# Kernel tuning notes

Hardware: AMD Instinct MI355X
Metric: run time of the kernel (lower is better)

The kernel has to match this reference:

```python
import jax, jax.numpy as jnp
import numpy as np

B, T, N, C = 2, 3, 6, 16            # batch, time steps, cameras, frustum channels
FD, FH, FW = 48, 24, 64             # frustum depth bins, feature height, width
GX, GY, GZ = 100, 100, 8            # voxel grid size (X, Y, Z)
PC_MIN = np.array([-50.0, -50.0, -3.0], np.float32)
PC_MAX = np.array([50.0, 50.0, 5.0], np.float32)
D_MIN, D_MAX = 2.0, 46.8            # uniform depth discretization (UD)
OUT_CH = 40


def setup_inputs() -> dict:
    key = jax.random.key(0)
    ks = jax.random.split(key, 8)
    frustum_features = jax.random.normal(ks[0], (B, T, N, C, FD, FH, FW), jnp.float32)
    # camera looks along world +x so voxel points land in front of the camera
    base_rt = jnp.array([[0., -1., 0., 0.],
                         [0., 0., -1., 0.],
                         [1., 0., 0., 0.],
                         [0., 0., 0., 1.]], jnp.float32)
    RT = base_rt + 0.02 * jax.random.normal(ks[1], (B, T, N, 4, 4), jnp.float32)
    K = jnp.array([[32., 0., FW / 2.], [0., 32., FH / 2.], [0., 0., 1.]], jnp.float32)
    intrins = K + 0.1 * jax.random.normal(ks[2], (B, 3, 3), jnp.float32)
    DoF = jnp.eye(4, dtype=jnp.float32) + 0.01 * jax.random.normal(ks[3], (B, T, 4, 4), jnp.float32)
    W_N = 0.05 * jax.random.normal(ks[4], (OUT_CH, N * C), jnp.float32)
    b_N = jnp.zeros((OUT_CH,), jnp.float32)
    W_T = 0.05 * jax.random.normal(ks[5], (OUT_CH, T * OUT_CH), jnp.float32)
    b_T = jnp.zeros((OUT_CH,), jnp.float32)
    return {"frustum_features": frustum_features, "RT": RT, "intrins": intrins,
            "DoF": DoF, "W_N": W_N, "b_N": b_N, "W_T": W_T, "b_T": b_T}


def _grid_sample_3d(feat, grid):
    """Trilinear grid_sample. feat [M,C,D,H,W], grid [M,A,B2,C3,3] with
    normalized (x->W, y->H, z->D) coords, align_corners=True, zeros padding."""
    def one(f, g):
        _, Dd, Hh, Ww = f.shape
        ix = (g[..., 0] + 1.) * 0.5 * (Ww - 1)
        iy = (g[..., 1] + 1.) * 0.5 * (Hh - 1)
        iz = (g[..., 2] + 1.) * 0.5 * (Dd - 1)
        x0 = jnp.floor(ix); y0 = jnp.floor(iy); z0 = jnp.floor(iz)
        wx1 = ix - x0; wy1 = iy - y0; wz1 = iz - z0
        wx0 = 1. - wx1; wy0 = 1. - wy1; wz0 = 1. - wz1

        def corner(zf, yf, xf, w):
            valid = ((xf >= 0) & (xf <= Ww - 1) & (yf >= 0) & (yf <= Hh - 1)
                     & (zf >= 0) & (zf <= Dd - 1))
            zi = jnp.clip(zf, 0, Dd - 1).astype(jnp.int32)
            yi = jnp.clip(yf, 0, Hh - 1).astype(jnp.int32)
            xi = jnp.clip(xf, 0, Ww - 1).astype(jnp.int32)
            v = f[:, zi, yi, xi]                       # [C, A, B2, C3]
            return v * (w * valid)[None]

        return (corner(z0, y0, x0, wz0 * wy0 * wx0)
                + corner(z0, y0, x0 + 1, wz0 * wy0 * wx1)
                + corner(z0, y0 + 1, x0, wz0 * wy1 * wx0)
                + corner(z0, y0 + 1, x0 + 1, wz0 * wy1 * wx1)
                + corner(z0 + 1, y0, x0, wz1 * wy0 * wx0)
                + corner(z0 + 1, y0, x0 + 1, wz1 * wy0 * wx1)
                + corner(z0 + 1, y0 + 1, x0, wz1 * wy1 * wx0)
                + corner(z0 + 1, y0 + 1, x0 + 1, wz1 * wy1 * wx1))
    return jax.vmap(one)(feat, grid)


def _frustum_grid(intrins, RT):
    """Project voxel centers into (u, v, depth-bin) frustum coords, normalized to [-1,1]."""
    vs = (PC_MAX - PC_MIN) / np.array([GX, GY, GZ], np.float32)
    xs = PC_MIN[0] + (np.arange(GX, dtype=np.float32) + 0.5) * vs[0]
    ys = PC_MIN[1] + (np.arange(GY, dtype=np.float32) + 0.5) * vs[1]
    zs = PC_MIN[2] + (np.arange(GZ, dtype=np.float32) + 0.5) * vs[2]
    xx, yy, zz = np.meshgrid(xs, ys, zs, indexing='ij')
    pts = jnp.asarray(np.stack([xx, yy, zz, np.ones_like(xx)], -1))  # [GX,GY,GZ,4]
    cam = jnp.einsum('btnij,xyzj->btnxyzi', RT, pts)[..., :3]
    proj = jnp.einsum('bij,btnxyzj->btnxyzi', intrins, cam)
    zc = jnp.maximum(proj[..., 2], 1e-5)
    u = proj[..., 0] / zc
    v = proj[..., 1] / zc
    dbin = (proj[..., 2] - D_MIN) / ((D_MAX - D_MIN) / FD)
    gx = 2. * u / (FW - 1) - 1.
    gy = 2. * v / (FH - 1) - 1.
    gz = 2. * dbin / (FD - 1) - 1.
    return jnp.stack([gx, gy, gz], -1)  # [B,T,N,GX,GY,GZ,3]


def _affine_grid(theta, Dp, Hp, Wp):
    zs = np.linspace(-1., 1., Dp, dtype=np.float32)
    ys = np.linspace(-1., 1., Hp, dtype=np.float32)
    xs = np.linspace(-1., 1., Wp, dtype=np.float32)
    zz, yy, xx = np.meshgrid(zs, ys, xs, indexing='ij')
    base = jnp.asarray(np.stack([xx, yy, zz, np.ones_like(xx)], -1))  # [Dp,Hp,Wp,4]
    return jnp.einsum('bij,dhwj->bdhwi', theta, base)


def reference(frustum_features, RT, intrins, DoF, W_N, b_N, W_T, b_T):
    # --- per-time, per-camera frustum -> voxel sampling (batched over B*T*N) ---
    grids = _frustum_grid(intrins, RT)                                  # [B,T,N,GX,GY,GZ,3]
    feats = frustum_features.reshape(B * T * N, C, FD, FH, FW)
    gflat = grids.reshape(B * T * N, GX, GY, GZ, 3)
    vox = _grid_sample_3d(feats, gflat).reshape(B, T, N, C, GX, GY, GZ)
    vox = vox.transpose(0, 1, 2, 3, 4, 6, 5)                            # [B,T,N,C,GX,GZ,GY] (Y/Z swap from original permute)
    vox = vox.reshape(B, T, N * C, GX, GZ, GY)
    # --- Conv3DCollapse_N: 1x1x1 conv over cameras x channels + ReLU ---
    h = jax.nn.relu(jnp.einsum('oc,btcxyz->btoxyz', W_N, vox)
                    + b_N[None, None, :, None, None, None])             # [B,T,40,GX,GZ,GY]
    # --- cumulative temporal warp (trilinear grid_sample with affine pose grids) ---
    theta = DoF[:, :, 0:3, :]                                           # [B,T,3,4]
    bottom = jnp.broadcast_to(jnp.array([0., 0., 0., 1.], jnp.float32), (B, T, 1, 4))
    M4 = jnp.concatenate([theta, bottom], axis=2)                       # [B,T,4,4]
    Dp, Hp, Wp = GX, GZ, GY
    cum = jnp.broadcast_to(jnp.eye(4, dtype=jnp.float32), (B, 4, 4))
    outs = [None] * T
    for t in range(T - 1, -1, -1):                                      # small fixed T=3
        if t < T - 1:
            cum = jnp.einsum('bij,bjk->bik', M4[:, t], cum)
        g = _affine_grid(cum[:, :3, :], Dp, Hp, Wp)
        outs[t] = _grid_sample_3d(h[:, t], g)
    warped = jnp.stack(outs, axis=1)                                    # [B,T,40,Dp,Hp,Wp]
    flat = warped.reshape(B, T * OUT_CH, Dp, Hp, Wp)
    # --- Conv3DCollapse_T: 1x1x1 conv over time x channels + ReLU ---
    return jax.nn.relu(jnp.einsum('oc,bcxyz->boxyz', W_T, flat)
                       + b_T[None, :, None, None, None])
```

## Files before the change

### kernel.cpp

```cpp
#include <hip/hip_runtime.h>

#define NB 2
#define NT 3
#define NCAM 6
#define NC 16
#define FD 48
#define FH 24
#define FW 64
#define GX 100
#define GY 100
#define GZ 8
#define OC 40
#define NVOX (GX * GY * GZ)
#define FSZ (FD * FH * FW)
#define CAMSZ (NC * FSZ)
#define BTSZ (NCAM * CAMSZ)
#define HSZ ((size_t)NB * NT * OC * NVOX)
#define FT_ELEMS ((size_t)NB * NT * NCAM * FSZ * NC)

static __device__ __forceinline__ unsigned short f2bf_rne(float x) {
    unsigned int u = __float_as_uint(x);
    unsigned int r = (u + 0x7fffu + ((u >> 16) & 1u)) >> 16;
    return (unsigned short)r;
}
static __device__ __forceinline__ float bf_lo(unsigned int u) {
    return __uint_as_float(u << 16);
}
static __device__ __forceinline__ float bf_hi(unsigned int u) {
    return __uint_as_float(u & 0xffff0000u);
}

static __device__ __forceinline__ int xcd_swizzle(int bid, int nwg) {
    int xcd = bid & 7;
    int local = bid >> 3;
    int q = nwg >> 3, r = nwg & 7;
    return (xcd < r ? xcd * (q + 1) : r * (q + 1) + (xcd - r) * q) + local;
}

static __device__ __forceinline__ void do_setup(
    int tid, const float* __restrict__ RT, const float* __restrict__ intrins,
    const float* __restrict__ DoF, float* __restrict__ P,
    float* __restrict__ theta) {
    if (tid < NB * NT * NCAM) {
        int bt = tid / NCAM;
        int b = bt / NT;
        const float* I3 = intrins + b * 9;
        const float* R = RT + (size_t)tid * 16;
        float* Pp = P + tid * 12;
        for (int r = 0; r < 3; ++r)
            for (int c = 0; c < 4; ++c) {
                float s = 0.f;
                for (int k = 0; k < 3; ++k) s += I3[r * 3 + k] * R[k * 4 + c];
                Pp[r * 4 + c] = s;
            }
    }
    if (tid >= 64 && tid < 64 + NB) {
        int b = tid - 64;
        const float* D0 = DoF + (size_t)(b * NT + 0) * 16;
        const float* D1 = DoF + (size_t)(b * NT + 1) * 16;
        float* th = theta + (size_t)b * NT * 12;
        for (int i = 0; i < 12; ++i) th[2 * 12 + i] = 0.f;
        th[2 * 12 + 0] = 1.f; th[2 * 12 + 5] = 1.f; th[2 * 12 + 10] = 1.f;
        for (int i = 0; i < 12; ++i) th[1 * 12 + i] = D1[i];
        for (int r = 0; r < 3; ++r)
            for (int c = 0; c < 4; ++c) {
                float s = (c == 3) ? D0[r * 4 + 3] : 0.f;
                for (int k = 0; k < 3; ++k) s += D0[r * 4 + k] * D1[k * 4 + c];
                th[0 * 12 + r * 4 + c] = s;
            }
    }
}

__global__ void setup_kernel(const float* __restrict__ RT,
                             const float* __restrict__ intrins,
                             const float* __restrict__ DoF,
                             float* __restrict__ P,
                             float* __restrict__ theta) {
    do_setup(threadIdx.x, RT, intrins, DoF, P, theta);
}

template <typename FT>
__global__ __launch_bounds__(256) void transpose_feat(
    const float* __restrict__ feat, FT* __restrict__ ft,
    const float* __restrict__ RT, const float* __restrict__ intrins,
    const float* __restrict__ DoF, float* __restrict__ P,
    float* __restrict__ theta) {
    if (blockIdx.x == 0) do_setup(threadIdx.x, RT, intrins, DoF, P, theta);
    size_t tid = (size_t)blockIdx.x * 256 + threadIdx.x;
    int pos = (int)(tid % FSZ);
    int btn = (int)(tid / FSZ);
    const float* src = feat + (size_t)btn * CAMSZ + pos;
    float v[NC];
#pragma unroll
    for (int c = 0; c < NC; ++c) v[c] = src[(size_t)c * FSZ];
    if constexpr (sizeof(FT) == 4) {
        float4* dst = reinterpret_cast<float4*>(
            (float*)ft + ((size_t)btn * FSZ + pos) * NC);
#pragma unroll
        for (int q = 0; q < 4; ++q)
            dst[q] = make_float4(v[4 * q], v[4 * q + 1], v[4 * q + 2], v[4 * q + 3]);
    } else {
        unsigned int packed[8];
#pragma unroll
        for (int j = 0; j < 8; ++j)
            packed[j] = (unsigned int)f2bf_rne(v[2 * j]) |
                        ((unsigned int)f2bf_rne(v[2 * j + 1]) << 16);
        uint4* dst = reinterpret_cast<uint4*>(
            (unsigned short*)ft + ((size_t)btn * FSZ + pos) * NC);
        dst[0] = make_uint4(packed[0], packed[1], packed[2], packed[3]);
        dst[1] = make_uint4(packed[4], packed[5], packed[6], packed[7]);
    }
}

template <typename FT, bool CHLAST>
__global__ __launch_bounds__(256) void sample_mlp1(
    const float* __restrict__ feat,
    const FT* __restrict__ ft,
    const float* __restrict__ P,
    const float* __restrict__ W_N,
    const float* __restrict__ b_N,
    const float* __restrict__ W_T,
    unsigned short* __restrict__ g) {
    int tid = blockIdx.x * 256 + threadIdx.x;
    int vid = tid % NVOX;
    int bt = __builtin_amdgcn_readfirstlane(tid / NVOX);
    int gy = vid % GY;
    int r2 = vid / GY;
    int gz = r2 % GZ;
    int gx = r2 / GZ;
    float X = (float)gx - 49.5f;
    float Y = (float)gy - 49.5f;
    float Z = (float)gz - 2.5f;

    float acc[OC];
#pragma unroll
    for (int o = 0; o < OC; ++o) acc[o] = b_N[o];

    for (int n = 0; n < NCAM; ++n) {
        const float* Pp = P + (bt * NCAM + n) * 12;
        float px = Pp[0] * X + Pp[1] * Y + Pp[2] * Z + Pp[3];
        float py = Pp[4] * X + Pp[5] * Y + Pp[6] * Z + Pp[7];
        float pz = Pp[8] * X + Pp[9] * Y + Pp[10] * Z + Pp[11];
        float zc = fmaxf(pz, 1e-5f);
        float ix = px / zc;
        float iy = py / zc;
        float iz = (pz - 2.0f) * (48.0f / 44.8f);

        bool cam_valid = (ix > -1.f) & (ix < (float)FW) &
                         (iy > -1.f) & (iy < (float)FH) &
                         (iz > -1.f) & (iz < (float)FD);
        if (!cam_valid) continue;

        float x0 = floorf(ix), y0 = floorf(iy), z0 = floorf(iz);
        float wx1 = ix - x0, wy1 = iy - y0, wz1 = iz - z0;
        float wx0 = 1.f - wx1, wy0 = 1.f - wy1, wz0 = 1.f - wz1;

        float w8[8];
        int off8[8];
#pragma unroll
        for (int k = 0; k < 8; ++k) {
            float xf = x0 + (float)(k & 1);
            float yf = y0 + (float)((k >> 1) & 1);
            float zf = z0 + (float)(k >> 2);
            bool valid = (xf >= 0.f) & (xf <= (float)(FW - 1)) &
                         (yf >= 0.f) & (yf <= (float)(FH - 1)) &
                         (zf >= 0.f) & (zf <= (float)(FD - 1));
            int xi = (int)fminf(fmaxf(xf, 0.f), (float)(FW - 1));
            int yi = (int)fminf(fmaxf(yf, 0.f), (float)(FH - 1));
            int zi = (int)fminf(fmaxf(zf, 0.f), (float)(FD - 1));
            float w = ((k & 1) ? wx1 : wx0) * (((k >> 1) & 1) ? wy1 : wy0) *
                      ((k >> 2) ? wz1 : wz0);
            w8[k] = valid ? w : 0.f;
            off8[k] = (zi * FH + yi) * FW + xi;
        }

        float s[NC];
#pragma unroll
        for (int c = 0; c < NC; ++c) s[c] = 0.f;

        if constexpr (CHLAST) {
            const size_t camBase = (size_t)(bt * NCAM + n) * FSZ;
            if constexpr (sizeof(FT) == 4) {
#pragma unroll
                for (int k = 0; k < 8; ++k) {
                    float w = w8[k];
                    const float4* cp = reinterpret_cast<const float4*>(
                        (const float*)ft + (camBase + (size_t)off8[k]) * NC);
#pragma unroll
                    for (int q = 0; q < 4; ++q) {
                        float4 v = cp[q];
                        s[4 * q + 0] = fmaf(w, v.x, s[4 * q + 0]);
                        s[4 * q + 1] = fmaf(w, v.y, s[4 * q + 1]);
                        s[4 * q + 2] = fmaf(w, v.z, s[4 * q + 2]);
                        s[4 * q + 3] = fmaf(w, v.w, s[4 * q + 3]);
                    }
                }
            } else {
#pragma unroll
                for (int k = 0; k < 8; ++k) {
                    float w = w8[k];
                    const uint4* cp = reinterpret_cast<const uint4*>(
                        (const unsigned short*)ft + (camBase + (size_t)off8[k]) * NC);
                    uint4 a = cp[0], b2 = cp[1];
                    unsigned int uu[8] = {a.x, a.y, a.z, a.w, b2.x, b2.y, b2.z, b2.w};
#pragma unroll
                    for (int j = 0; j < 8; ++j) {
                        s[2 * j + 0] = fmaf(w, bf_lo(uu[j]), s[2 * j + 0]);
                        s[2 * j + 1] = fmaf(w, bf_hi(uu[j]), s[2 * j + 1]);
                    }
                }
            }
        } else {
            const float* fn = feat + (size_t)bt * BTSZ + (size_t)n * CAMSZ;
#pragma unroll
            for (int c = 0; c < NC; ++c) {
                const float* fc = fn + (size_t)c * FSZ;
                float v = 0.f;
#pragma unroll
                for (int k = 0; k < 8; ++k) v = fmaf(w8[k], fc[off8[k]], v);
                s[c] = v;
            }
        }

#pragma unroll
        for (int o = 0; o < OC; ++o) {
            const float4* w4 =
                reinterpret_cast<const float4*>(W_N + o * (NCAM * NC) + n * NC);
#pragma unroll
            for (int q = 0; q < 4; ++q) {
                float4 w = w4[q];
                acc[o] = fmaf(w.x, s[4 * q + 0], acc[o]);
                acc[o] = fmaf(w.y, s[4 * q + 1], acc[o]);
                acc[o] = fmaf(w.z, s[4 * q + 2], acc[o]);
                acc[o] = fmaf(w.w, s[4 * q + 3], acc[o]);
            }
        }
    }

#pragma unroll
    for (int o = 0; o < OC; ++o) acc[o] = fmaxf(acc[o], 0.f);

    const int t = bt % NT;
    const float* Wtb = W_T + t * OC;
    uint4* d4 = reinterpret_cast<uint4*>(
        g + ((size_t)bt * NVOX + (size_t)vid) * OC);
#pragma unroll
    for (int grp = 0; grp < 5; ++grp) {
        float g8[8];
#pragma unroll
        for (int j = 0; j < 8; ++j) {
            const float4* w4 = reinterpret_cast<const float4*>(
                Wtb + (size_t)(grp * 8 + j) * (NT * OC));
            float s0 = 0.f;
#pragma unroll
            for (int q = 0; q < 10; ++q) {
                float4 w = w4[q];
                s0 = fmaf(w.x, acc[4 * q + 0], s0);
                s0 = fmaf(w.y, acc[4 * q + 1], s0);
                s0 = fmaf(w.z, acc[4 * q + 2], s0);
                s0 = fmaf(w.w, acc[4 * q + 3], s0);
            }
            g8[j] = s0;
        }
        unsigned int u0 = (unsigned int)f2bf_rne(g8[0]) |
                          ((unsigned int)f2bf_rne(g8[1]) << 16);
        unsigned int u1 = (unsigned int)f2bf_rne(g8[2]) |
                          ((unsigned int)f2bf_rne(g8[3]) << 16);
        unsigned int u2 = (unsigned int)f2bf_rne(g8[4]) |
                          ((unsigned int)f2bf_rne(g8[5]) << 16);
        unsigned int u3 = (unsigned int)f2bf_rne(g8[6]) |
                          ((unsigned int)f2bf_rne(g8[7]) << 16);
        d4[grp] = make_uint4(u0, u1, u2, u3);
    }
}

__global__ __launch_bounds__(256) void warp_mlp2(
    const unsigned short* __restrict__ g,
    const float* __restrict__ theta,
    const float* __restrict__ b_T,
    float* __restrict__ out) {
    int bid = xcd_swizzle(blockIdx.x, gridDim.x);
    int tid = bid * 256 + threadIdx.x;
    int vid = tid % NVOX;
    int b = __builtin_amdgcn_readfirstlane(tid / NVOX);
    int w_ = vid % GY;
    int r2 = vid / GY;
    int h_ = r2 % GZ;
    int d_ = r2 / GZ;

    float xg = -1.f + 2.f * (float)w_ / 99.f;
    float yg = -1.f + 2.f * (float)h_ / 7.f;
    float zg = -1.f + 2.f * (float)d_ / 99.f;

    float sval[OC];
#pragma unroll
    for (int o = 0; o < OC; ++o) sval[o] = b_T[o];

    for (int t = 0; t < 2; ++t) {
        const float* th = theta + (b * NT + t) * 12;
        float g0 = th[0] * xg + th[1] * yg + th[2] * zg + th[3];
        float g1 = th[4] * xg + th[5] * yg + th[6] * zg + th[7];
        float g2 = th[8] * xg + th[9] * yg + th[10] * zg + th[11];
        float ix = (g0 + 1.f) * 0.5f * 99.f;
        float iy = (g1 + 1.f) * 0.5f * 7.f;
        float iz = (g2 + 1.f) * 0.5f * 99.f;
        float x0 = floorf(ix), y0 = floorf(iy), z0 = floorf(iz);
        float wx1 = ix - x0, wy1 = iy - y0, wz1 = iz - z0;
        float wx0 = 1.f - wx1, wy0 = 1.f - wy1, wz0 = 1.f - wz1;

        float w8[8];
        int off8[8];
#pragma unroll
        for (int k = 0; k < 8; ++k) {
            float xf = x0 + (float)(k & 1);
            float yf = y0 + (float)((k >> 1) & 1);
            float zf = z0 + (float)(k >> 2);
            bool valid = (xf >= 0.f) & (xf <= 99.f) &
                         (yf >= 0.f) & (yf <= 7.f) &
                         (zf >= 0.f) & (zf <= 99.f);
            int xi = (int)fminf(fmaxf(xf, 0.f), 99.f);
            int yi = (int)fminf(fmaxf(yf, 0.f), 7.f);
            int zi = (int)fminf(fmaxf(zf, 0.f), 99.f);
            float w = ((k & 1) ? wx1 : wx0) * (((k >> 1) & 1) ? wy1 : wy0) *
                      ((k >> 2) ? wz1 : wz0);
            w8[k] = valid ? w : 0.f;
            off8[k] = (zi * GZ + yi) * GY + xi;
        }

        const unsigned short* hb = g + (size_t)(b * NT + t) * NVOX * OC;
#pragma unroll
        for (int k = 0; k < 8; ++k) {
            float w = w8[k];
            const uint4* cp =
                reinterpret_cast<const uint4*>(hb + (size_t)off8[k] * OC);
            uint4 a0 = cp[0], a1 = cp[1], a2 = cp[2], a3 = cp[3], a4 = cp[4];
            unsigned int uu[20] = {a0.x, a0.y, a0.z, a0.w, a1.x, a1.y, a1.z, a1.w,
                                   a2.x, a2.y, a2.z, a2.w, a3.x, a3.y, a3.z, a3.w,
                                   a4.x, a4.y, a4.z, a4.w};
#pragma unroll
            for (int j = 0; j < 20; ++j) {
                sval[2 * j + 0] = fmaf(w, bf_lo(uu[j]), sval[2 * j + 0]);
                sval[2 * j + 1] = fmaf(w, bf_hi(uu[j]), sval[2 * j + 1]);
            }
        }
    }

    {
        const uint4* cp = reinterpret_cast<const uint4*>(
            g + ((size_t)(b * NT + 2) * NVOX + (size_t)vid) * OC);
        uint4 a0 = cp[0], a1 = cp[1], a2 = cp[2], a3 = cp[3], a4 = cp[4];
        unsigned int uu[20] = {a0.x, a0.y, a0.z, a0.w, a1.x, a1.y, a1.z, a1.w,
                               a2.x, a2.y, a2.z, a2.w, a3.x, a3.y, a3.z, a3.w,
                               a4.x, a4.y, a4.z, a4.w};
#pragma unroll
        for (int j = 0; j < 20; ++j) {
            sval[2 * j + 0] += bf_lo(uu[j]);
            sval[2 * j + 1] += bf_hi(uu[j]);
        }
    }

    float* op = out + (size_t)b * OC * NVOX + vid;
#pragma unroll
    for (int o = 0; o < OC; ++o) op[(size_t)o * NVOX] = fmaxf(sval[o], 0.f);
}

extern "C" void kernel_launch(void* const* d_in, const int* in_sizes, int n_in,
                              void* d_out, int out_size, void* d_ws, size_t ws_size,
                              hipStream_t stream) {
    const float* frustum = (const float*)d_in[0];
    const float* RT      = (const float*)d_in[1];
    const float* intrins = (const float*)d_in[2];
    const float* DoF     = (const float*)d_in[3];
    const float* W_N     = (const float*)d_in[4];
    const float* b_N     = (const float*)d_in[5];
    const float* W_T     = (const float*)d_in[6];
    const float* b_T     = (const float*)d_in[7];
    float* out = (float*)d_out;

    const size_t ft_f32  = FT_ELEMS * sizeof(float);
    const size_t ft_bf16 = FT_ELEMS * sizeof(unsigned short);
    const size_t h_bytes = HSZ * sizeof(unsigned short);
    const size_t small = 4096;

    char* base = (char*)d_ws;
    int mode;
    size_t ft_bytes;
    if (ws_size >= ft_f32 + h_bytes + small) { mode = 0; ft_bytes = ft_f32; }
    else if (ws_size >= ft_bf16 + h_bytes + small) { mode = 1; ft_bytes = ft_bf16; }
    else { mode = 2; ft_bytes = 0; }

    size_t ft_al = (ft_bytes + 255) & ~(size_t)255;
    void* ft_buf = base;
    unsigned short* g_buf = (unsigned short*)(base + ft_al);
    float* P_buf = (float*)(base + ft_al + ((h_bytes + 255) & ~(size_t)255));
    float* th_buf = P_buf + NB * NT * NCAM * 12;

    const int tr_blocks = (NB * NT * NCAM * FSZ) / 256;
    const int n1_blocks = (NB * NT * NVOX) / 256;
    const int n2_blocks = (NB * NVOX) / 256;

    if (mode == 0) {
        transpose_feat<float><<<tr_blocks, 256, 0, stream>>>(
            frustum, (float*)ft_buf, RT, intrins, DoF, P_buf, th_buf);
        sample_mlp1<float, true><<<n1_blocks, 256, 0, stream>>>(
            frustum, (const float*)ft_buf, P_buf, W_N, b_N, W_T, g_buf);
    } else if (mode == 1) {
        transpose_feat<unsigned short><<<tr_blocks, 256, 0, stream>>>(
            frustum, (unsigned short*)ft_buf, RT, intrins, DoF, P_buf, th_buf);
        sample_mlp1<unsigned short, true><<<n1_blocks, 256, 0, stream>>>(
            frustum, (const unsigned short*)ft_buf, P_buf, W_N, b_N, W_T, g_buf);
    } else {
        setup_kernel<<<1, 128, 0, stream>>>(RT, intrins, DoF, P_buf, th_buf);
        sample_mlp1<float, false><<<n1_blocks, 256, 0, stream>>>(
            frustum, (const float*)nullptr, P_buf, W_N, b_N, W_T, g_buf);
    }

    warp_mlp2<<<n2_blocks, 256, 0, stream>>>(g_buf, th_buf, b_T, out);
}
```

Baseline: 414.1 us.

## Always use bf16 channel-last features and short-circuit voxels seen by no camera

Removes the fp32 channel-last feature path so the transpose always writes bf16, halving the intermediate buffer and the gather traffic in the sampling kernel. The setup step also precomputes, per batch and time, the temporal-MLP output for a voxel with no valid camera (W_T times relu(b_N)). Voxels that miss every camera copy this constant instead of running the 40x40 matmul. The cost is extra bf16 rounding of features where fp32 was used before, and some divergence inside wavefronts where only some voxels are valid.

```diff
diff --git a/kernel.cpp b/kernel.cpp
--- a/kernel.cpp
+++ b/kernel.cpp
@@ -39,8 +39,9 @@
 
 static __device__ __forceinline__ void do_setup(
     int tid, const float* __restrict__ RT, const float* __restrict__ intrins,
-    const float* __restrict__ DoF, float* __restrict__ P,
-    float* __restrict__ theta) {
+    const float* __restrict__ DoF, const float* __restrict__ W_T,
+    const float* __restrict__ b_N, float* __restrict__ P,
+    float* __restrict__ theta, unsigned short* __restrict__ g_const) {
     if (tid < NB * NT * NCAM) {
         int bt = tid / NCAM;
         int b = bt / NT;
@@ -69,23 +70,38 @@
                 th[0 * 12 + r * 4 + c] = s;
             }
     }
+    if (tid >= 96 && tid < 96 + NB * NT) {
+        int bt = tid - 96;
+        int t = bt % NT;
+        unsigned short* gc = g_const + (size_t)bt * OC;
+        for (int o = 0; o < OC; ++o) {
+            float s = 0.f;
+            const float* wrow = W_T + (size_t)o * (NT * OC) + t * OC;
+            for (int c = 0; c < OC; ++c) s += wrow[c] * fmaxf(b_N[c], 0.f);
+            gc[o] = f2bf_rne(s);
+        }
+    }
 }
 
 __global__ void setup_kernel(const float* __restrict__ RT,
                              const float* __restrict__ intrins,
                              const float* __restrict__ DoF,
+                             const float* __restrict__ W_T,
+                             const float* __restrict__ b_N,
                              float* __restrict__ P,
-                             float* __restrict__ theta) {
-    do_setup(threadIdx.x, RT, intrins, DoF, P, theta);
-}
-
-template <typename FT>
+                             float* __restrict__ theta,
+                             unsigned short* __restrict__ g_const) {
+    do_setup(threadIdx.x, RT, intrins, DoF, W_T, b_N, P, theta, g_const);
+}
+
 __global__ __launch_bounds__(256) void transpose_feat(
-    const float* __restrict__ feat, FT* __restrict__ ft,
+    const float* __restrict__ feat, unsigned short* __restrict__ ft,
     const float* __restrict__ RT, const float* __restrict__ intrins,
-    const float* __restrict__ DoF, float* __restrict__ P,
-    float* __restrict__ theta) {
-    if (blockIdx.x == 0) do_setup(threadIdx.x, RT, intrins, DoF, P, theta);
+    const float* __restrict__ DoF, const float* __restrict__ W_T,
+    const float* __restrict__ b_N, float* __restrict__ P,
+    float* __restrict__ theta, unsigned short* __restrict__ g_const) {
+    if (blockIdx.x == 0)
+        do_setup(threadIdx.x, RT, intrins, DoF, W_T, b_N, P, theta, g_const);
     size_t tid = (size_t)blockIdx.x * 256 + threadIdx.x;
     int pos = (int)(tid % FSZ);
     int btn = (int)(tid / FSZ);
@@ -93,33 +109,25 @@
     float v[NC];
 #pragma unroll
     for (int c = 0; c < NC; ++c) v[c] = src[(size_t)c * FSZ];
-    if constexpr (sizeof(FT) == 4) {
-        float4* dst = reinterpret_cast<float4*>(
-            (float*)ft + ((size_t)btn * FSZ + pos) * NC);
-#pragma unroll
-        for (int q = 0; q < 4; ++q)
-            dst[q] = make_float4(v[4 * q], v[4 * q + 1], v[4 * q + 2], v[4 * q + 3]);
-    } else {
-        unsigned int packed[8];
-#pragma unroll
-        for (int j = 0; j < 8; ++j)
-            packed[j] = (unsigned int)f2bf_rne(v[2 * j]) |
-                        ((unsigned int)f2bf_rne(v[2 * j + 1]) << 16);
-        uint4* dst = reinterpret_cast<uint4*>(
-            (unsigned short*)ft + ((size_t)btn * FSZ + pos) * NC);
-        dst[0] = make_uint4(packed[0], packed[1], packed[2], packed[3]);
-        dst[1] = make_uint4(packed[4], packed[5], packed[6], packed[7]);
-    }
-}
-
-template <typename FT, bool CHLAST>
+    unsigned int packed[8];
+#pragma unroll
+    for (int j = 0; j < 8; ++j)
+        packed[j] = (unsigned int)f2bf_rne(v[2 * j]) |
+                    ((unsigned int)f2bf_rne(v[2 * j + 1]) << 16);
+    uint4* dst = reinterpret_cast<uint4*>(ft + ((size_t)btn * FSZ + pos) * NC);
+    dst[0] = make_uint4(packed[0], packed[1], packed[2], packed[3]);
+    dst[1] = make_uint4(packed[4], packed[5], packed[6], packed[7]);
+}
+
+template <bool CHLAST>
 __global__ __launch_bounds__(256) void sample_mlp1(
     const float* __restrict__ feat,
-    const FT* __restrict__ ft,
+    const unsigned short* __restrict__ ft,
     const float* __restrict__ P,
     const float* __restrict__ W_N,
     const float* __restrict__ b_N,
     const float* __restrict__ W_T,
+    const unsigned short* __restrict__ g_const,
     unsigned short* __restrict__ g) {
     int tid = blockIdx.x * 256 + threadIdx.x;
     int vid = tid % NVOX;
@@ -132,9 +140,14 @@
     float Y = (float)gy - 49.5f;
     float Z = (float)gz - 2.5f;
 
+    uint4* d4 = reinterpret_cast<uint4*>(
+        g + ((size_t)bt * NVOX + (size_t)vid) * OC);
+
     float acc[OC];
 #pragma unroll
     for (int o = 0; o < OC; ++o) acc[o] = b_N[o];
+
+    bool any_valid = false;
 
     for (int n = 0; n < NCAM; ++n) {
         const float* Pp = P + (bt * NCAM + n) * 12;
@@ -150,6 +163,7 @@
                          (iy > -1.f) & (iy < (float)FH) &
                          (iz > -1.f) & (iz < (float)FD);
         if (!cam_valid) continue;
+        any_valid = true;
 
         float x0 = floorf(ix), y0 = floorf(iy), z0 = floorf(iz);
         float wx1 = ix - x0, wy1 = iy - y0, wz1 = iz - z0;
@@ -180,34 +194,17 @@
 
         if constexpr (CHLAST) {
             const size_t camBase = (size_t)(bt * NCAM + n) * FSZ;
-            if constexpr (sizeof(FT) == 4) {
-#pragma unroll
-                for (int k = 0; k < 8; ++k) {
-                    float w = w8[k];
-                    const float4* cp = reinterpret_cast<const float4*>(
-                        (const float*)ft + (camBase + (size_t)off8[k]) * NC);
-#pragma unroll
-                    for (int q = 0; q < 4; ++q) {
-                        float4 v = cp[q];
-                        s[4 * q + 0] = fmaf(w, v.x, s[4 * q + 0]);
-                        s[4 * q + 1] = fmaf(w, v.y, s[4 * q + 1]);
-                        s[4 * q + 2] = fmaf(w, v.z, s[4 * q + 2]);
-                        s[4 * q + 3] = fmaf(w, v.w, s[4 * q + 3]);
-                    }
-                }
-            } else {
-#pragma unroll
-                for (int k = 0; k < 8; ++k) {
-                    float w = w8[k];
-                    const uint4* cp = reinterpret_cast<const uint4*>(
-                        (const unsigned short*)ft + (camBase + (size_t)off8[k]) * NC);
-                    uint4 a = cp[0], b2 = cp[1];
-                    unsigned int uu[8] = {a.x, a.y, a.z, a.w, b2.x, b2.y, b2.z, b2.w};
-#pragma unroll
-                    for (int j = 0; j < 8; ++j) {
-                        s[2 * j + 0] = fmaf(w, bf_lo(uu[j]), s[2 * j + 0]);
-                        s[2 * j + 1] = fmaf(w, bf_hi(uu[j]), s[2 * j + 1]);
-                    }
+#pragma unroll
+            for (int k = 0; k < 8; ++k) {
+                float w = w8[k];
+                const uint4* cp = reinterpret_cast<const uint4*>(
+                    ft + (camBase + (size_t)off8[k]) * NC);
+                uint4 a = cp[0], b2 = cp[1];
+                unsigned int uu[8] = {a.x, a.y, a.z, a.w, b2.x, b2.y, b2.z, b2.w};
+#pragma unroll
+                for (int j = 0; j < 8; ++j) {
+                    s[2 * j + 0] = fmaf(w, bf_lo(uu[j]), s[2 * j + 0]);
+                    s[2 * j + 1] = fmaf(w, bf_hi(uu[j]), s[2 * j + 1]);
                 }
             }
         } else {
@@ -237,13 +234,19 @@
         }
     }
 
+    if (!any_valid) {
+        const uint4* gc = reinterpret_cast<const uint4*>(
+            g_const + (size_t)bt * OC);
+        uint4 r0 = gc[0], r1 = gc[1], r2_ = gc[2], r3 = gc[3], r4 = gc[4];
+        d4[0] = r0; d4[1] = r1; d4[2] = r2_; d4[3] = r3; d4[4] = r4;
+        return;
+    }
+
 #pragma unroll
     for (int o = 0; o < OC; ++o) acc[o] = fmaxf(acc[o], 0.f);
 
     const int t = bt % NT;
     const float* Wtb = W_T + t * OC;
-    uint4* d4 = reinterpret_cast<uint4*>(
-        g + ((size_t)bt * NVOX + (size_t)vid) * OC);
 #pragma unroll
     for (int grp = 0; grp < 5; ++grp) {
         float g8[8];
@@ -377,42 +380,35 @@
     const float* b_T     = (const float*)d_in[7];
     float* out = (float*)d_out;
 
-    const size_t ft_f32  = FT_ELEMS * sizeof(float);
-    const size_t ft_bf16 = FT_ELEMS * sizeof(unsigned short);
-    const size_t h_bytes = HSZ * sizeof(unsigned short);
+    const size_t ft_bytes = FT_ELEMS * sizeof(unsigned short);
+    const size_t g_bytes  = HSZ * sizeof(unsigned short);
     const size_t small = 4096;
 
     char* base = (char*)d_ws;
-    int mode;
-    size_t ft_bytes;
-    if (ws_size >= ft_f32 + h_bytes + small) { mode = 0; ft_bytes = ft_f32; }
-    else if (ws_size >= ft_bf16 + h_bytes + small) { mode = 1; ft_bytes = ft_bf16; }
-    else { mode = 2; ft_bytes = 0; }
-
-    size_t ft_al = (ft_bytes + 255) & ~(size_t)255;
-    void* ft_buf = base;
+    bool use_ft = ws_size >= ft_bytes + g_bytes + small;
+
+    size_t ft_al = use_ft ? ((ft_bytes + 255) & ~(size_t)255) : 0;
+    unsigned short* ft_buf = (unsigned short*)base;
     unsigned short* g_buf = (unsigned short*)(base + ft_al);
-    float* P_buf = (float*)(base + ft_al + ((h_bytes + 255) & ~(size_t)255));
+    float* P_buf = (float*)(base + ft_al + ((g_bytes + 255) & ~(size_t)255));
     float* th_buf = P_buf + NB * NT * NCAM * 12;
+    unsigned short* gc_buf = (unsigned short*)(th_buf + NB * NT * 12);
 
     const int tr_blocks = (NB * NT * NCAM * FSZ) / 256;
     const int n1_blocks = (NB * NT * NVOX) / 256;
     const int n2_blocks = (NB * NVOX) / 256;
 
-    if (mode == 0) {
-        transpose_feat<float><<<tr_blocks, 256, 0, stream>>>(
-            frustum, (float*)ft_buf, RT, intrins, DoF, P_buf, th_buf);
-        sample_mlp1<float, true><<<n1_blocks, 256, 0, stream>>>(
-            frustum, (const float*)ft_buf, P_buf, W_N, b_N, W_T, g_buf);
-    } else if (mode == 1) {
-        transpose_feat<unsigned short><<<tr_blocks, 256, 0, stream>>>(
-            frustum, (unsigned short*)ft_buf, RT, intrins, DoF, P_buf, th_buf);
-        sample_mlp1<unsigned short, true><<<n1_blocks, 256, 0, stream>>>(
-            frustum, (const unsigned short*)ft_buf, P_buf, W_N, b_N, W_T, g_buf);
+    if (use_ft) {
+        transpose_feat<<<tr_blocks, 256, 0, stream>>>(
+            frustum, ft_buf, RT, intrins, DoF, W_T, b_N, P_buf, th_buf, gc_buf);
+        sample_mlp1<true><<<n1_blocks, 256, 0, stream>>>(
+            frustum, ft_buf, P_buf, W_N, b_N, W_T, gc_buf, g_buf);
     } else {
-        setup_kernel<<<1, 128, 0, stream>>>(RT, intrins, DoF, P_buf, th_buf);
-        sample_mlp1<float, false><<<n1_blocks, 256, 0, stream>>>(
-            frustum, (const float*)nullptr, P_buf, W_N, b_N, W_T, g_buf);
+        setup_kernel<<<1, 128, 0, stream>>>(
+            RT, intrins, DoF, W_T, b_N, P_buf, th_buf, gc_buf);
+        sample_mlp1<false><<<n1_blocks, 256, 0, stream>>>(
+            frustum, (const unsigned short*)nullptr, P_buf, W_N, b_N, W_T,
+            gc_buf, g_buf);
     }
 
     warp_mlp2<<<n2_blocks, 256, 0, stream>>>(g_buf, th_buf, b_T, out);
```

After: 388.6 us. -6.2%, faster.
